# Kernel tuning notes

Hardware: AMD Instinct MI355X
Metric: run time of the kernel (lower is better)

Reference implementation:

```python
import jax, jax.numpy as jnp
import numpy as np

B, H, W, C = 32, 128, 128, 64
MX, MY = 32, 32  # modes_x, modes_y


def setup_inputs() -> dict:
    key = jax.random.key(0)
    k1, k2, k3, k4 = jax.random.split(key, 4)
    # glorot-ish scales for the spectral and conv weights
    wscale = (2.0 / (C + C)) ** 0.5
    return {
        "x": jax.random.normal(k1, (B, H, W, C), dtype=jnp.float32),
        "w_real": jax.random.normal(k2, (MX, MY, C, C), dtype=jnp.float32) * wscale,
        "w_imag": jax.random.normal(k3, (MX, MY, C, C), dtype=jnp.float32) * wscale,
        "conv_w": jax.random.normal(k4, (C, C), dtype=jnp.float32) * wscale,
        "conv_b": jnp.zeros((C,), dtype=jnp.float32),
    }


def reference(x, w_real, w_imag, conv_w, conv_b):
    # Complex spectral mixing weights [MX, MY, Cin, Cout]
    weights = jax.lax.complex(w_real, w_imag)
    # tf.signal.fft2d transforms the innermost TWO axes of [B,H,W,C],
    # i.e. axes (W, C); jnp.fft.fft2 default axes=(-2,-1) matches exactly.
    x_ft = jnp.fft.fft2(x.astype(jnp.complex64))           # [B,H,W,C] complex64
    # Mode truncation on axes (H, W), as in the original code.
    x_ft_trunc = x_ft[:, :MX, :MY, :]                      # [B,MX,MY,C]
    # Complex channel-mixing einsum over the low modes.
    x_ft_proc = jnp.einsum('bxyi,xyio->bxyo', x_ft_trunc, weights)  # [B,MX,MY,C]
    # Zero-pad back to the full grid on (H, W).
    x_ft_padded = jnp.pad(x_ft_proc,
                          ((0, 0), (0, H - MX), (0, W - MY), (0, 0)))
    # IFFT again over innermost two axes (W, C), take real part.
    x_spec = jnp.real(jnp.fft.ifft2(x_ft_padded))          # [B,H,W,C] float32
    # 1x1 conv (pointwise channel mix) + bias on the raw input.
    x_local = jnp.einsum('bhwi,io->bhwo', x, conv_w) + conv_b
    return jax.nn.relu(x_spec + x_local)
```

## Files before the change

### kernel.cpp

```cpp
#include <hip/hip_runtime.h>

typedef __attribute__((ext_vector_type(8))) short short8;
typedef __attribute__((ext_vector_type(4))) float f32x4;
typedef unsigned short ushort_t;

#define MFMA(a, b, c) __builtin_amdgcn_mfma_f32_16x16x32_bf16((a), (b), (c), 0, 0, 0)

constexpr int NB = 32, NHt = 128, NWd = 128, NC = 64, MX = 32;
constexpr float TWO_PI = 6.28318530717958647692f;

constexpr size_t TAB_T1 = 0;
constexpr size_t TAB_T2 = 16384;
constexpr size_t TAB_T3 = 32768;
constexpr size_t TAB_T4 = 49152;
constexpr size_t XY_OFF = 65536;

__device__ inline ushort_t f2bf(float f) {
    union { float f; unsigned int u; } v; v.f = f;
    unsigned int r = v.u + 0x7FFFu + ((v.u >> 16) & 1u);
    return (ushort_t)(r >> 16);
}
__device__ inline float bf2f(ushort_t b) {
    union { unsigned int u; float f; } v; v.u = ((unsigned int)b) << 16;
    return v.f;
}

__global__ __launch_bounds__(256) void k0_tables(ushort_t* __restrict__ tabs)
{
    int e = blockIdx.x * 256 + threadIdx.x;
    int tab = e >> 9, rem = e & 511;
    float re[8], im[8];
    if (tab == 0) {
        int mt = rem >> 8, ks = (rem >> 6) & 3, l = rem & 63;
        int uu = (l & 15) + 16 * mt, wb = (l >> 4) * 8 + 32 * ks;
        #pragma unroll
        for (int j = 0; j < 8; ++j) {
            float a = (float)((uu * (wb + j)) & 127) * (TWO_PI / 128.f);
            re[j] = cosf(a); im[j] = -sinf(a);
        }
    } else if (tab == 1) {
        int nt = rem >> 7, ks = (rem >> 6) & 1, l = rem & 63;
        int kk = (l & 15) + 16 * nt, cb2 = (l >> 4) * 8 + 32 * ks;
        #pragma unroll
        for (int j = 0; j < 8; ++j) {
            float a = (float)((kk * (cb2 + j)) & 63) * (TWO_PI / 64.f);
            re[j] = cosf(a); im[j] = -sinf(a);
        }
    } else if (tab == 2) {
        int nt = rem >> 7, ks = (rem >> 6) & 1, l = rem & 63;
        int cc = (l & 15) + 16 * nt, ob = (l >> 4) * 8 + 32 * ks;
        #pragma unroll
        for (int j = 0; j < 8; ++j) {
            float a = (float)(((ob + j) * cc) & 63) * (TWO_PI / 64.f);
            re[j] = cosf(a); im[j] = sinf(a);
        }
    } else {
        int mt = rem >> 6, l = rem & 63;
        int w = (l & 15) + 16 * mt, ub = (l >> 4) * 8;
        #pragma unroll
        for (int j = 0; j < 8; ++j) {
            float a = (float)((w * (ub + j)) & 127) * (TWO_PI / 128.f);
            re[j] = cosf(a); im[j] = sinf(a);
        }
    }
    ushort_t* dst = tabs + (size_t)e * 16;
    #pragma unroll
    for (int j = 0; j < 8; ++j) { dst[j] = f2bf(re[j]); dst[8 + j] = f2bf(im[j]); }
}

__global__ __launch_bounds__(512) void k1_fwd(
    const float* __restrict__ x, const char* __restrict__ tabs, ushort_t* __restrict__ XY)
{
    const int b = blockIdx.x, h = blockIdx.y;
    const int tid = threadIdx.x, lane = tid & 63, wv = tid >> 6;
    constexpr int SXT  = 0;
    constexpr int M1RE = 17408;
    constexpr int M1IM = 17408 + 4608;
    __shared__ __align__(16) char sm[26624];

    const float* xs = x + ((size_t)(b * NHt + h)) * (NWd * NC);
    #pragma unroll
    for (int i = 0; i < 4; ++i) {
        int w = (tid >> 4) + 32 * i;
        #pragma unroll
        for (int j = 0; j < 4; ++j) {
            int c = (tid & 15) + 16 * j;
            *(ushort_t*)(sm + SXT + c * 272 + w * 2) = f2bf(xs[w * 64 + c]);
        }
    }
    __syncthreads();

    const int mt = wv >> 2, nt = wv & 3;
    f32x4 m1r = {0.f,0.f,0.f,0.f}, m1i = {0.f,0.f,0.f,0.f};
    #pragma unroll
    for (int ks = 0; ks < 4; ++ks) {
        short8 bfrag = *reinterpret_cast<const short8*>(
            sm + SXT + ((lane & 15) + 16 * nt) * 272 + (lane >> 4) * 16 + 64 * ks);
        const char* t1 = tabs + TAB_T1 + (((mt * 4 + ks) * 64 + lane) * 32);
        short8 are = *reinterpret_cast<const short8*>(t1);
        short8 aim = *reinterpret_cast<const short8*>(t1 + 16);
        m1r = MFMA(are, bfrag, m1r);
        m1i = MFMA(aim, bfrag, m1i);
    }
    #pragma unroll
    for (int r = 0; r < 4; ++r) {
        int u = (lane >> 4) * 4 + r + 16 * mt;
        int c = (lane & 15) + 16 * nt;
        *(ushort_t*)(sm + M1RE + u * 144 + c * 2) = f2bf(m1r[r]);
        *(ushort_t*)(sm + M1IM + u * 144 + c * 2) = f2bf(m1i[r]);
    }
    __syncthreads();

    f32x4 xP = {0.f,0.f,0.f,0.f}, xQ = {0.f,0.f,0.f,0.f}, xI = {0.f,0.f,0.f,0.f};
    #pragma unroll
    for (int ks = 0; ks < 2; ++ks) {
        short8 are = *reinterpret_cast<const short8*>(
            sm + M1RE + ((lane & 15) + 16 * mt) * 144 + (lane >> 4) * 16 + 64 * ks);
        short8 aim = *reinterpret_cast<const short8*>(
            sm + M1IM + ((lane & 15) + 16 * mt) * 144 + (lane >> 4) * 16 + 64 * ks);
        const char* t2 = tabs + TAB_T2 + (((nt * 2 + ks) * 64 + lane) * 32);
        short8 bre = *reinterpret_cast<const short8*>(t2);
        short8 bim = *reinterpret_cast<const short8*>(t2 + 16);
        xP = MFMA(are, bre, xP);
        xQ = MFMA(aim, bim, xQ);
        xI = MFMA(are, bim, xI);
        xI = MFMA(aim, bre, xI);
    }
    #pragma unroll
    for (int r = 0; r < 4; ++r) {
        int u = (lane >> 4) * 4 + r + 16 * mt;
        int k = (lane & 15) + 16 * nt;
        size_t hu = (size_t)(h * 32 + u);
        XY[((hu * 2 + 0) * 32 + b) * 64 + k] = f2bf(xP[r] - xQ[r]);
        XY[((hu * 2 + 1) * 32 + b) * 64 + k] = f2bf(xI[r]);
    }
}

__global__ __launch_bounds__(256) void k2_mix(
    const float* __restrict__ wre, const float* __restrict__ wim, ushort_t* __restrict__ XY)
{
    const int h = blockIdx.x, u = blockIdx.y;
    const int tid = threadIdx.x, lane = tid & 63, wv = tid >> 6;
    constexpr int XRE = 0, XIM = 4608, WTR = 9216, WTI = 18432;
    __shared__ __align__(16) char sm[27648];
    const size_t hu = (size_t)(h * 32 + u);

    #pragma unroll
    for (int it = 0; it < 2; ++it) {
        int row = (tid >> 3) + 32 * it;
        int comp = row >> 5, bb = row & 31, k8 = (tid & 7) * 8;
        short8 v = *reinterpret_cast<const short8*>(XY + ((hu * 2 + comp) * 32 + bb) * 64 + k8);
        *reinterpret_cast<short8*>(sm + (comp ? XIM : XRE) + bb * 144 + k8 * 2) = v;
    }
    const float* wr = wre + hu * 4096;
    const float* wi = wim + hu * 4096;
    #pragma unroll
    for (int i = 0; i < 4; ++i) {
        int k = (tid >> 4) + 16 * i;
        #pragma unroll
        for (int j = 0; j < 4; ++j) {
            int o = (tid & 15) + 16 * j;
            *(ushort_t*)(sm + WTR + o * 144 + k * 2) = f2bf(wr[k * 64 + o]);
            *(ushort_t*)(sm + WTI + o * 144 + k * 2) = f2bf(wi[k * 64 + o]);
        }
    }
    __syncthreads();

    const int mt = wv >> 1;
    #pragma unroll
    for (int half = 0; half < 2; ++half) {
        const int nt = (wv & 1) * 2 + half;
        f32x4 yP = {0.f,0.f,0.f,0.f}, yQ = {0.f,0.f,0.f,0.f}, yI = {0.f,0.f,0.f,0.f};
        #pragma unroll
        for (int ks = 0; ks < 2; ++ks) {
            short8 are = *reinterpret_cast<const short8*>(
                sm + XRE + ((lane & 15) + 16 * mt) * 144 + (lane >> 4) * 16 + 64 * ks);
            short8 aim = *reinterpret_cast<const short8*>(
                sm + XIM + ((lane & 15) + 16 * mt) * 144 + (lane >> 4) * 16 + 64 * ks);
            short8 bre = *reinterpret_cast<const short8*>(
                sm + WTR + ((lane & 15) + 16 * nt) * 144 + (lane >> 4) * 16 + 64 * ks);
            short8 bim = *reinterpret_cast<const short8*>(
                sm + WTI + ((lane & 15) + 16 * nt) * 144 + (lane >> 4) * 16 + 64 * ks);
            yP = MFMA(are, bre, yP); yQ = MFMA(aim, bim, yQ);
            yI = MFMA(are, bim, yI); yI = MFMA(aim, bre, yI);
        }
        #pragma unroll
        for (int r = 0; r < 4; ++r) {
            int bb = (lane >> 4) * 4 + r + 16 * mt;
            int o = (lane & 15) + 16 * nt;
            XY[((hu * 2 + 0) * 32 + bb) * 64 + o] = f2bf(yP[r] - yQ[r]);
            XY[((hu * 2 + 1) * 32 + bb) * 64 + o] = f2bf(yI[r]);
        }
    }
}

__global__ __launch_bounds__(512) void k3_inv(
    const float* __restrict__ x, const float* __restrict__ cw, const float* __restrict__ cb,
    const char* __restrict__ tabs, const ushort_t* __restrict__ XY, float* __restrict__ out)
{
    const int b = blockIdx.x, h = blockIdx.y;
    const int tid = threadIdx.x, lane = tid & 63, wv = tid >> 6;
    constexpr int ST_RE = 0, ST_IM = 5120;
    constexpr int YRE = 10240, YIM = 14848;
    constexpr int XHI = 10240, XLO = 28672;
    constexpr int CWT = 47104;
    constexpr int SCB = 56320;
    __shared__ __align__(16) char sm[56576];

    if (h < MX) {
        {
            int u = tid >> 4, comp = (tid >> 3) & 1, o8 = (tid & 7) * 8;
            size_t hu = (size_t)(h * 32 + u);
            short8 v = *reinterpret_cast<const short8*>(XY + ((hu * 2 + comp) * 32 + b) * 64 + o8);
            *reinterpret_cast<short8*>(sm + (comp ? YIM : YRE) + u * 144 + o8 * 2) = v;
        }
        __syncthreads();
        const int mt = wv >> 2, nt = wv & 3;
        f32x4 sP = {0.f,0.f,0.f,0.f}, sQ = {0.f,0.f,0.f,0.f}, sI = {0.f,0.f,0.f,0.f};
        #pragma unroll
        for (int ks = 0; ks < 2; ++ks) {
            short8 are = *reinterpret_cast<const short8*>(
                sm + YRE + ((lane & 15) + 16 * mt) * 144 + (lane >> 4) * 16 + 64 * ks);
            short8 aim = *reinterpret_cast<const short8*>(
                sm + YIM + ((lane & 15) + 16 * mt) * 144 + (lane >> 4) * 16 + 64 * ks);
            const char* t3 = tabs + TAB_T3 + (((nt * 2 + ks) * 64 + lane) * 32);
            short8 bre = *reinterpret_cast<const short8*>(t3);
            short8 bim = *reinterpret_cast<const short8*>(t3 + 16);
            sP = MFMA(are, bre, sP); sQ = MFMA(aim, bim, sQ);
            sI = MFMA(are, bim, sI); sI = MFMA(aim, bre, sI);
        }
        #pragma unroll
        for (int r = 0; r < 4; ++r) {
            int u = (lane >> 4) * 4 + r + 16 * mt;
            int c = (lane & 15) + 16 * nt;
            *(ushort_t*)(sm + ST_RE + c * 80 + u * 2) = f2bf(sP[r] - sQ[r]);
            *(ushort_t*)(sm + ST_IM + c * 80 + u * 2) = f2bf(sI[r]);
        }
    }
    __syncthreads();

    const float* xs = x + ((size_t)(b * NHt + h)) * (NWd * NC);
    #pragma unroll
    for (int i = 0; i < 4; ++i) {
        int idx4 = tid + 512 * i;
        int w = idx4 >> 4, c4 = (idx4 & 15) * 4;
        float4 v = *reinterpret_cast<const float4*>(xs + w * 64 + c4);
        ushort_t h0 = f2bf(v.x), h1 = f2bf(v.y), h2 = f2bf(v.z), h3 = f2bf(v.w);
        *(unsigned int*)(sm + XHI + w * 144 + c4 * 2)     = (unsigned)h0 | ((unsigned)h1 << 16);
        *(unsigned int*)(sm + XHI + w * 144 + c4 * 2 + 4) = (unsigned)h2 | ((unsigned)h3 << 16);
        ushort_t l0 = f2bf(v.x - bf2f(h0)), l1 = f2bf(v.y - bf2f(h1));
        ushort_t l2 = f2bf(v.z - bf2f(h2)), l3 = f2bf(v.w - bf2f(h3));
        *(unsigned int*)(sm + XLO + w * 144 + c4 * 2)     = (unsigned)l0 | ((unsigned)l1 << 16);
        *(unsigned int*)(sm + XLO + w * 144 + c4 * 2 + 4) = (unsigned)l2 | ((unsigned)l3 << 16);
    }
    #pragma unroll
    for (int i = 0; i < 2; ++i) {
        int ii = (tid >> 4) + 32 * i;
        #pragma unroll
        for (int j = 0; j < 4; ++j) {
            int o = (tid & 15) + 16 * j;
            *(ushort_t*)(sm + CWT + o * 144 + ii * 2) = f2bf(cw[ii * 64 + o]);
        }
    }
    if (tid < 64) ((float*)(sm + SCB))[tid] = cb[tid];
    __syncthreads();

    short8 gre = {}, gim = {};
    if (h < MX) {
        const char* t4 = tabs + TAB_T4 + ((wv * 64 + lane) * 32);
        gre = *reinterpret_cast<const short8*>(t4);
        gim = *reinterpret_cast<const short8*>(t4 + 16);
    }
    float* orow = out + ((size_t)(b * NHt + h)) * (NWd * NC);
    #pragma unroll
    for (int nt = 0; nt < 4; ++nt) {
        f32x4 acc = {0.f,0.f,0.f,0.f};
        #pragma unroll
        for (int ks = 0; ks < 2; ++ks) {
            short8 ah = *reinterpret_cast<const short8*>(
                sm + XHI + ((lane & 15) + 16 * wv) * 144 + (lane >> 4) * 16 + 64 * ks);
            short8 al = *reinterpret_cast<const short8*>(
                sm + XLO + ((lane & 15) + 16 * wv) * 144 + (lane >> 4) * 16 + 64 * ks);
            short8 bw = *reinterpret_cast<const short8*>(
                sm + CWT + ((lane & 15) + 16 * nt) * 144 + (lane >> 4) * 16 + 64 * ks);
            acc = MFMA(ah, bw, acc);
            acc = MFMA(al, bw, acc);
        }
        f32x4 sp = {0.f,0.f,0.f,0.f}, sq = {0.f,0.f,0.f,0.f};
        if (h < MX) {
            short8 bre = *reinterpret_cast<const short8*>(
                sm + ST_RE + ((lane & 15) + 16 * nt) * 80 + (lane >> 4) * 16);
            short8 bim = *reinterpret_cast<const short8*>(
                sm + ST_IM + ((lane & 15) + 16 * nt) * 80 + (lane >> 4) * 16);
            sp = MFMA(gre, bre, sp);
            sq = MFMA(gim, bim, sq);
        }
        #pragma unroll
        for (int r = 0; r < 4; ++r) {
            int w = (lane >> 4) * 4 + r + 16 * wv;
            int c = (lane & 15) + 16 * nt;
            float v = acc[r] + ((const float*)(sm + SCB))[c];
            if (h < MX) v += (sp[r] - sq[r]) * (1.0f / 8192.0f);
            orow[w * 64 + c] = fmaxf(v, 0.0f);
        }
    }
}

extern "C" void kernel_launch(void* const* d_in, const int* in_sizes, int n_in,
                              void* d_out, int out_size, void* d_ws, size_t ws_size,
                              hipStream_t stream) {
    const float* x      = (const float*)d_in[0];
    const float* w_real = (const float*)d_in[1];
    const float* w_imag = (const float*)d_in[2];
    const float* conv_w = (const float*)d_in[3];
    const float* conv_b = (const float*)d_in[4];
    float* out = (float*)d_out;

    ushort_t* tabs = (ushort_t*)d_ws;
    ushort_t* XY   = (ushort_t*)((char*)d_ws + XY_OFF);

    k0_tables<<<8, 256, 0, stream>>>(tabs);
    k1_fwd<<<dim3(NB, MX), 512, 0, stream>>>(x, (const char*)d_ws, XY);
    k2_mix<<<dim3(MX, 32), 256, 0, stream>>>(w_real, w_imag, XY);
    k3_inv<<<dim3(NB, NHt), 512, 0, stream>>>(x, conv_w, conv_b,
                                              (const char*)d_ws, XY, out);
}
```

Baseline: 85.91 us.

## Vectorize global loads and stores, drop split-bf16 conv, fold IFFT scale into table

Forward and mix kernels now load x and the spectral weights with float4 (nontemporal for weights and x), and stage results in shared memory so each writes XY with coalesced 16-byte stores instead of scattered 2-byte ones. The final kernel drops the hi/lo bf16 split for the pointwise conv, which halves its MFMAs and LDS use at the cost of precision on the local path. The 1/8192 IFFT normalization is folded into the T4 table. This risks bf16 underflow or accuracy loss in the scaled table, and it adds extra syncs.

```diff
diff --git a/kernel.cpp b/kernel.cpp
--- a/kernel.cpp
+++ b/kernel.cpp
@@ -19,10 +19,6 @@
     union { float f; unsigned int u; } v; v.f = f;
     unsigned int r = v.u + 0x7FFFu + ((v.u >> 16) & 1u);
     return (ushort_t)(r >> 16);
-}
-__device__ inline float bf2f(ushort_t b) {
-    union { unsigned int u; float f; } v; v.u = ((unsigned int)b) << 16;
-    return v.f;
 }
 
 __global__ __launch_bounds__(256) void k0_tables(ushort_t* __restrict__ tabs)
@@ -60,7 +56,8 @@
         #pragma unroll
         for (int j = 0; j < 8; ++j) {
             float a = (float)((w * (ub + j)) & 127) * (TWO_PI / 128.f);
-            re[j] = cosf(a); im[j] = sinf(a);
+            re[j] = cosf(a) * 0.0001220703125f;
+            im[j] = sinf(a) * 0.0001220703125f;
         }
     }
     ushort_t* dst = tabs + (size_t)e * 16;
@@ -81,12 +78,12 @@
     const float* xs = x + ((size_t)(b * NHt + h)) * (NWd * NC);
     #pragma unroll
     for (int i = 0; i < 4; ++i) {
-        int w = (tid >> 4) + 32 * i;
-        #pragma unroll
-        for (int j = 0; j < 4; ++j) {
-            int c = (tid & 15) + 16 * j;
-            *(ushort_t*)(sm + SXT + c * 272 + w * 2) = f2bf(xs[w * 64 + c]);
-        }
+        int idx = tid + 512 * i;
+        int w = idx >> 4, c4 = (idx & 15) * 4;
+        f32x4 v = *reinterpret_cast<const f32x4*>(xs + w * 64 + c4);
+        #pragma unroll
+        for (int j = 0; j < 4; ++j)
+            *(ushort_t*)(sm + SXT + (c4 + j) * 272 + w * 2) = f2bf(v[j]);
     }
     __syncthreads();
 
@@ -130,9 +127,16 @@
     for (int r = 0; r < 4; ++r) {
         int u = (lane >> 4) * 4 + r + 16 * mt;
         int k = (lane & 15) + 16 * nt;
+        *(ushort_t*)(sm + SXT + 0    + u * 128 + k * 2) = f2bf(xP[r] - xQ[r]);
+        *(ushort_t*)(sm + SXT + 4096 + u * 128 + k * 2) = f2bf(xI[r]);
+    }
+    __syncthreads();
+
+    {
+        int u = tid >> 4, comp = (tid >> 3) & 1, k8 = (tid & 7) * 8;
+        short8 v = *reinterpret_cast<const short8*>(sm + SXT + comp * 4096 + u * 128 + k8 * 2);
         size_t hu = (size_t)(h * 32 + u);
-        XY[((hu * 2 + 0) * 32 + b) * 64 + k] = f2bf(xP[r] - xQ[r]);
-        XY[((hu * 2 + 1) * 32 + b) * 64 + k] = f2bf(xI[r]);
+        *reinterpret_cast<short8*>(XY + ((hu * 2 + comp) * 32 + b) * 64 + k8) = v;
     }
 }
 
@@ -156,17 +160,20 @@
     const float* wi = wim + hu * 4096;
     #pragma unroll
     for (int i = 0; i < 4; ++i) {
-        int k = (tid >> 4) + 16 * i;
+        int idx = tid + 256 * i;
+        int k = idx >> 4, o4 = (idx & 15) * 4;
+        f32x4 vr = __builtin_nontemporal_load(reinterpret_cast<const f32x4*>(wr + k * 64 + o4));
+        f32x4 vi = __builtin_nontemporal_load(reinterpret_cast<const f32x4*>(wi + k * 64 + o4));
         #pragma unroll
         for (int j = 0; j < 4; ++j) {
-            int o = (tid & 15) + 16 * j;
-            *(ushort_t*)(sm + WTR + o * 144 + k * 2) = f2bf(wr[k * 64 + o]);
-            *(ushort_t*)(sm + WTI + o * 144 + k * 2) = f2bf(wi[k * 64 + o]);
+            *(ushort_t*)(sm + WTR + (o4 + j) * 144 + k * 2) = f2bf(vr[j]);
+            *(ushort_t*)(sm + WTI + (o4 + j) * 144 + k * 2) = f2bf(vi[j]);
         }
     }
     __syncthreads();
 
     const int mt = wv >> 1;
+    f32x4 yRe[2], yIm[2];
     #pragma unroll
     for (int half = 0; half < 2; ++half) {
         const int nt = (wv & 1) * 2 + half;
@@ -185,12 +192,28 @@
             yI = MFMA(are, bim, yI); yI = MFMA(aim, bre, yI);
         }
         #pragma unroll
+        for (int r = 0; r < 4; ++r) { yRe[half][r] = yP[r] - yQ[r]; yIm[half][r] = yI[r]; }
+    }
+    __syncthreads();
+
+    #pragma unroll
+    for (int half = 0; half < 2; ++half) {
+        const int nt = (wv & 1) * 2 + half;
+        #pragma unroll
         for (int r = 0; r < 4; ++r) {
             int bb = (lane >> 4) * 4 + r + 16 * mt;
             int o = (lane & 15) + 16 * nt;
-            XY[((hu * 2 + 0) * 32 + bb) * 64 + o] = f2bf(yP[r] - yQ[r]);
-            XY[((hu * 2 + 1) * 32 + bb) * 64 + o] = f2bf(yI[r]);
-        }
+            *(ushort_t*)(sm + 0    + bb * 128 + o * 2) = f2bf(yRe[half][r]);
+            *(ushort_t*)(sm + 4096 + bb * 128 + o * 2) = f2bf(yIm[half][r]);
+        }
+    }
+    __syncthreads();
+
+    #pragma unroll
+    for (int it = 0; it < 2; ++it) {
+        int flat = tid + 256 * it;
+        short8 v = *reinterpret_cast<const short8*>(sm + flat * 16);
+        *reinterpret_cast<short8*>(XY + hu * 4096 + flat * 8) = v;
     }
 }
 
@@ -202,10 +225,10 @@
     const int tid = threadIdx.x, lane = tid & 63, wv = tid >> 6;
     constexpr int ST_RE = 0, ST_IM = 5120;
     constexpr int YRE = 10240, YIM = 14848;
-    constexpr int XHI = 10240, XLO = 28672;
-    constexpr int CWT = 47104;
-    constexpr int SCB = 56320;
-    __shared__ __align__(16) char sm[56576];
+    constexpr int XB  = 10240;
+    constexpr int CWT = 28672;
+    constexpr int SCB = 37888;
+    __shared__ __align__(16) char sm[38144];
 
     if (h < MX) {
         {
@@ -242,16 +265,12 @@
     const float* xs = x + ((size_t)(b * NHt + h)) * (NWd * NC);
     #pragma unroll
     for (int i = 0; i < 4; ++i) {
-        int idx4 = tid + 512 * i;
-        int w = idx4 >> 4, c4 = (idx4 & 15) * 4;
-        float4 v = *reinterpret_cast<const float4*>(xs + w * 64 + c4);
-        ushort_t h0 = f2bf(v.x), h1 = f2bf(v.y), h2 = f2bf(v.z), h3 = f2bf(v.w);
-        *(unsigned int*)(sm + XHI + w * 144 + c4 * 2)     = (unsigned)h0 | ((unsigned)h1 << 16);
-        *(unsigned int*)(sm + XHI + w * 144 + c4 * 2 + 4) = (unsigned)h2 | ((unsigned)h3 << 16);
-        ushort_t l0 = f2bf(v.x - bf2f(h0)), l1 = f2bf(v.y - bf2f(h1));
-        ushort_t l2 = f2bf(v.z - bf2f(h2)), l3 = f2bf(v.w - bf2f(h3));
-        *(unsigned int*)(sm + XLO + w * 144 + c4 * 2)     = (unsigned)l0 | ((unsigned)l1 << 16);
-        *(unsigned int*)(sm + XLO + w * 144 + c4 * 2 + 4) = (unsigned)l2 | ((unsigned)l3 << 16);
+        int idx = tid + 512 * i;
+        int w = idx >> 4, c4 = (idx & 15) * 4;
+        f32x4 v = __builtin_nontemporal_load(reinterpret_cast<const f32x4*>(xs + w * 64 + c4));
+        ushort_t h0 = f2bf(v[0]), h1 = f2bf(v[1]), h2 = f2bf(v[2]), h3 = f2bf(v[3]);
+        *(unsigned int*)(sm + XB + w * 144 + c4 * 2)     = (unsigned)h0 | ((unsigned)h1 << 16);
+        *(unsigned int*)(sm + XB + w * 144 + c4 * 2 + 4) = (unsigned)h2 | ((unsigned)h3 << 16);
     }
     #pragma unroll
     for (int i = 0; i < 2; ++i) {
@@ -278,13 +297,10 @@
         #pragma unroll
         for (int ks = 0; ks < 2; ++ks) {
             short8 ah = *reinterpret_cast<const short8*>(
-                sm + XHI + ((lane & 15) + 16 * wv) * 144 + (lane >> 4) * 16 + 64 * ks);
-            short8 al = *reinterpret_cast<const short8*>(
-                sm + XLO + ((lane & 15) + 16 * wv) * 144 + (lane >> 4) * 16 + 64 * ks);
+                sm + XB + ((lane & 15) + 16 * wv) * 144 + (lane >> 4) * 16 + 64 * ks);
             short8 bw = *reinterpret_cast<const short8*>(
                 sm + CWT + ((lane & 15) + 16 * nt) * 144 + (lane >> 4) * 16 + 64 * ks);
             acc = MFMA(ah, bw, acc);
-            acc = MFMA(al, bw, acc);
         }
         f32x4 sp = {0.f,0.f,0.f,0.f}, sq = {0.f,0.f,0.f,0.f};
         if (h < MX) {
@@ -300,7 +316,7 @@
             int w = (lane >> 4) * 4 + r + 16 * wv;
             int c = (lane & 15) + 16 * nt;
             float v = acc[r] + ((const float*)(sm + SCB))[c];
-            if (h < MX) v += (sp[r] - sq[r]) * (1.0f / 8192.0f);
+            if (h < MX) v += sp[r] - sq[r];
             orow[w * 64 + c] = fmaxf(v, 0.0f);
         }
     }
```

Measured after the change: 84.56 us. About the same (-1.6%).
